# Kernel optimization log

Hardware: AMD Instinct MI355X
Metric: run time of the kernel (lower is better)

## Reference

```python
import jax, jax.numpy as jnp
import numpy as np

B, N_VEC, D, C, N_W, N_CLASS, VOCAB = 16, 4096, 256, 256, 12, 10, 32
N_LINKS = N_W + 1


def _chord_cols(n_vec, n_links):
    # cols[i] = [i, (i+2^0)%n, (i+2^1)%n, ..., (i+2^(L-2))%n]
    i = np.arange(n_vec)[:, None]
    offs = np.concatenate([[0], 2 ** np.arange(n_links - 1)])[None, :]
    return ((i + offs) % n_vec).astype(np.int32)


def setup_inputs() -> dict:
    key = jax.random.key(0)
    ks = jax.random.split(key, 16)
    s = 0.02
    return {
        "tokens": jax.random.randint(ks[0], (B, N_VEC), 0, VOCAB),
        "cols": jnp.asarray(_chord_cols(N_VEC, N_LINKS)),
        "emb": jax.random.normal(ks[1], (VOCAB, D), jnp.float32) * s,
        "pos_emb": jax.random.normal(ks[2], (N_VEC, D), jnp.float32) * s,
        "g_w1": jax.random.normal(ks[3], (D, C), jnp.float32) * s,
        "g_b1": jnp.zeros((C,), jnp.float32),
        "g_w2": jax.random.normal(ks[4], (C, C), jnp.float32) * s,
        "g_b2": jnp.zeros((C,), jnp.float32),
        "fs_w1": jax.random.normal(ks[5], (N_W, D, D), jnp.float32) * s,
        "fs_b1": jnp.zeros((N_W, D), jnp.float32),
        "fs_w2": jax.random.normal(ks[6], (N_W, D, N_LINKS), jnp.float32) * s,
        "fs_b2": jnp.zeros((N_W, N_LINKS), jnp.float32),
        "fin_w": jax.random.normal(ks[7], (C, N_CLASS), jnp.float32) * s,
        "fin_b": jnp.zeros((N_CLASS,), jnp.float32),
    }


def reference(tokens, cols, emb, pos_emb, g_w1, g_b1, g_w2, g_b2,
              fs_w1, fs_b1, fs_w2, fs_b2, fin_w, fin_b):
    # token + positional embedding: [B, N, D]
    data = emb[tokens] + pos_emb[None, :, :]
    # g MLP -> V: [B, N, C]   (torch GELU = exact erf)
    V = jax.nn.gelu(data @ g_w1 + g_b1, approximate=False) @ g_w2 + g_b2
    res = V
    n_w = fs_w1.shape[0]
    for m in range(n_w):
        # per-edge weights: [B, N, L]
        W = jax.nn.gelu(data @ fs_w1[m] + fs_b1[m], approximate=False) @ fs_w2[m] + fs_b2[m]
        # chord spmm: V[b,i] = sum_l W[b,i,l] * V[b, cols[i,l]]
        Vg = V[:, cols, :]                       # [B, N, L, C]
        V = jnp.einsum('bnl,bnlc->bnc', W, Vg) + res
    cls = V[:, 0, :]                             # CLS pooling
    return cls @ fin_w + fin_b
```

## Files before the change

### kernel.cpp

```cpp
#include <hip/hip_runtime.h>
#include <hip/hip_bf16.h>
#include <math.h>

namespace {

constexpr int Bb   = 16;
constexpr int Nv   = 4096;
constexpr int NW   = 12;
constexpr int NL   = 13;
constexpr int NCLS = 10;
constexpr int BN   = Bb * Nv;

typedef __attribute__((ext_vector_type(8))) short short8;
typedef __attribute__((ext_vector_type(4))) float float4_t;

__device__ __forceinline__ float gelu_poly(float x) {
    float u = x * x;
    float p = fmaf(u, fmaf(u, fmaf(u, -2.374656431e-3f, 1.994711402e-2f),
                           -1.329807601e-1f), 7.978845608e-1f);
    return x * fmaf(x * p, 0.5f, 0.5f);
}
__device__ __forceinline__ float bflo(unsigned int u) {
    return __builtin_bit_cast(float, u << 16);
}
__device__ __forceinline__ float bfhi(unsigned int u) {
    return __builtin_bit_cast(float, u & 0xffff0000u);
}
__device__ __forceinline__ unsigned int f2bf(float f) {
    unsigned int x = __builtin_bit_cast(unsigned int, f);
    x += 0x7fff + ((x >> 16) & 1);
    return x >> 16;
}
__device__ __forceinline__ unsigned short f2bf16(float f) {
    return __builtin_bit_cast(unsigned short, __float2bfloat16(f));
}
__device__ __forceinline__ void gload16(const unsigned short* g, unsigned short* l) {
    __builtin_amdgcn_global_load_lds(
        (const __attribute__((address_space(1))) void*)g,
        (__attribute__((address_space(3))) void*)l, 16, 0, 0);
}
__device__ __forceinline__ int xcd_swz(int bid) {
    return (bid & 7) * 128 + (bid >> 3);
}


__global__ __launch_bounds__(256) void xbf_kernel(
    const int* __restrict__ tokens,
    const float* __restrict__ emb,
    const float* __restrict__ pos,
    unsigned int* __restrict__ Xbf)
{
    int i  = blockIdx.x * 256 + threadIdx.x;
    int p  = i & 127;
    int bn = i >> 7;
    int n  = bn & (Nv - 1);
    int t  = tokens[bn];
    const float2* e2 = (const float2*)(emb + (size_t)t * 256);
    const float2* p2 = (const float2*)(pos + (size_t)n * 256);
    float2 a = e2[p], b = p2[p];
    Xbf[i] = f2bf(a.x + b.x) | (f2bf(a.y + b.y) << 16);
}

__global__ __launch_bounds__(256) void wt_kernel(
    const float* __restrict__ g_w1,
    const float* __restrict__ g_w2,
    const float* __restrict__ fs_w1,
    const float* __restrict__ fs_w2,
    unsigned short* __restrict__ WT,
    unsigned short* __restrict__ W2T)
{
    int bid = blockIdx.x;
    int t = threadIdx.x;
    if (bid < 14 * 16) {
        int mat = bid >> 4;
        int k0  = (bid & 15) * 16;
        const float* src = (mat == 0) ? g_w1
                         : (mat == 1) ? g_w2
                         : fs_w1 + (size_t)(mat - 2) * 65536;
        unsigned short tmp[16];
#pragma unroll
        for (int j = 0; j < 16; ++j)
            tmp[j] = (unsigned short)f2bf(src[(size_t)(k0 + j) * 256 + t]);
        unsigned short* dst = WT + ((size_t)mat * 256 + t) * 256 + k0;
#pragma unroll
        for (int j = 0; j < 16; ++j) dst[j] = tmp[j];
    } else {
        int m = bid - 224;
        const float* src = fs_w2 + (size_t)m * 256 * NL;
        unsigned short* dst = W2T + (size_t)m * 4096;
#pragma unroll
        for (int i = 0; i < 16; ++i) {
            int idx = t + i * 256;
            int n = idx >> 8, k = idx & 255;
            dst[idx] = (n < NL) ? (unsigned short)f2bf(src[(size_t)k * NL + n]) : 0;
        }
    }
}

__device__ __forceinline__ void gemm1_core(
    const unsigned short* __restrict__ Xg,
    const unsigned short* __restrict__ Wg,
    int row0, int tid,
    unsigned short* Xs,
    unsigned short* Wls,
    float4_t acc[4][4])
{
    const int w = tid >> 6, lane = tid & 63;
    const int wr = w >> 2, wc = w & 3;
    const int l15 = lane & 15, lg = lane >> 4;

    for (int k0 = 0; k0 < 256; k0 += 64) {
#pragma unroll
        for (int i = 0; i < 2; ++i) {
            int slotb = i * 512 + w * 64;
            int slot = slotb + lane;
            int row = slot >> 3, pu = slot & 7, lu = pu ^ (row & 7);
            gload16(Xg + (size_t)(row0 + row) * 256 + k0 + lu * 8, Xs + slotb * 8);
        }
#pragma unroll
        for (int i = 0; i < 4; ++i) {
            int slotb = i * 512 + w * 64;
            int slot = slotb + lane;
            int n = slot >> 3, pu = slot & 7, lu = pu ^ (n & 7);
            gload16(Wg + (size_t)n * 256 + k0 + lu * 8, Wls + slotb * 8);
        }
        __syncthreads();

#pragma unroll
        for (int ks = 0; ks < 2; ++ks) {
            short8 a[4], b[4];
#pragma unroll
            for (int fr = 0; fr < 4; ++fr) {
                int r = wr * 64 + fr * 16 + l15;
                int off = r * 128 + (((lg + ks * 4) ^ (l15 & 7)) << 4);
                a[fr] = *(const short8*)((const char*)Xs + off);
            }
#pragma unroll
            for (int nt = 0; nt < 4; ++nt) {
                int n = wc * 64 + nt * 16 + l15;
                int off = n * 128 + (((lg + ks * 4) ^ (l15 & 7)) << 4);
                b[nt] = *(const short8*)((const char*)Wls + off);
            }
#pragma unroll
            for (int fr = 0; fr < 4; ++fr)
#pragma unroll
                for (int nt = 0; nt < 4; ++nt)
                    acc[fr][nt] = __builtin_amdgcn_mfma_f32_16x16x32_bf16(
                        a[fr], b[nt], acc[fr][nt], 0, 0, 0);
        }
        __syncthreads();
    }
}

template<bool GELU>
__global__ __launch_bounds__(512) void gemm_act_kernel(
    const unsigned short* __restrict__ X,
    const unsigned short* __restrict__ WT,
    const float* __restrict__ bias,
    unsigned short* __restrict__ Y)
{
    __shared__ __align__(128) unsigned char smem[49152];
    unsigned short* Xs  = (unsigned short*)smem;
    unsigned short* Wls = (unsigned short*)(smem + 16384);

    const int row0 = ((blockIdx.x & 7) * 64 + (blockIdx.x >> 3)) * 128;
    const int tid  = threadIdx.x;
    const int w = tid >> 6, lane = tid & 63;
    const int wr = w >> 2, wc = w & 3;
    const int l15 = lane & 15, lg = lane >> 4;

    float4_t acc[4][4];
#pragma unroll
    for (int fr = 0; fr < 4; ++fr)
#pragma unroll
        for (int nt = 0; nt < 4; ++nt) acc[fr][nt] = (float4_t)0.f;

    gemm1_core(X, WT, row0, tid, Xs, Wls, acc);

#pragma unroll
    for (int nt = 0; nt < 4; ++nt) {
        int c = wc * 64 + nt * 16 + l15;
        float bv = bias[c];
#pragma unroll
        for (int fr = 0; fr < 4; ++fr)
#pragma unroll
            for (int reg = 0; reg < 4; ++reg) {
                float v = acc[fr][nt][reg] + bv;
                if (GELU) v = gelu_poly(v);
                Y[(size_t)(row0 + wr * 64 + fr * 16 + lg * 4 + reg) * 256 + c]
                    = f2bf16(v);
            }
    }
}

__global__ __launch_bounds__(512) void fsmlp_kernel(
    const unsigned short* __restrict__ X,
    const unsigned short* __restrict__ WT,
    const unsigned short* __restrict__ W2T,
    const float* __restrict__ fs_b1,
    const float* __restrict__ fs_b2,
    float* __restrict__ Wall)
{
    __shared__ __align__(128) unsigned char smem[65536];
    unsigned short* Xs  = (unsigned short*)smem;
    unsigned short* Wls = (unsigned short*)(smem + 16384);
    unsigned short* Hs  = (unsigned short*)smem;

    const int bid  = (blockIdx.x & 7) * 768 + (blockIdx.x >> 3);
    const int m    = bid % 12;
    const int row0 = (bid / 12) * 128;
    const int tid  = threadIdx.x;
    const int w = tid >> 6, lane = tid & 63;
    const int wr = w >> 2, wc = w & 3;
    const int l15 = lane & 15, lg = lane >> 4;

    const unsigned short* Wg   = WT + (size_t)(2 + m) * 65536;
    const unsigned short* W2Tm = W2T + (size_t)m * 4096;
    const float* b1m = fs_b1 + (size_t)m * 256;
    const float* b2m = fs_b2 + (size_t)m * NL;
    float* Wallm = Wall + (size_t)m * BN * NL;

    float4_t acc[4][4];
#pragma unroll
    for (int fr = 0; fr < 4; ++fr)
#pragma unroll
        for (int nt = 0; nt < 4; ++nt) acc[fr][nt] = (float4_t)0.f;

    gemm1_core(X, Wg, row0, tid, Xs, Wls, acc);

    short8 b2[8];
#pragma unroll
    for (int kc = 0; kc < 8; ++kc)
        b2[kc] = *(const short8*)(W2Tm + l15 * 256 + kc * 32 + lg * 8);

#pragma unroll
    for (int nt = 0; nt < 4; ++nt) {
        int c = wc * 64 + nt * 16 + l15;
        float bv = b1m[c];
        int cu = c >> 3, cl = c & 7;
#pragma unroll
        for (int fr = 0; fr < 4; ++fr)
#pragma unroll
            for (int reg = 0; reg < 4; ++reg) {
                int row = wr * 64 + fr * 16 + lg * 4 + reg;
                Hs[row * 256 + ((cu ^ (row & 7)) << 3) + cl] =
                    f2bf16(gelu_poly(acc[fr][nt][reg] + bv));
            }
    }
    __syncthreads();

    float4_t wacc = (float4_t)0.f;
#pragma unroll
    for (int kc = 0; kc < 8; ++kc) {
        int ua = (((kc * 4 + lg) ^ (l15 & 7)) << 3);
        short8 a = *(const short8*)(Hs + (w * 16 + l15) * 256 + ua);
        wacc = __builtin_amdgcn_mfma_f32_16x16x32_bf16(a, b2[kc], wacc, 0, 0, 0);
    }
    if (l15 < NL) {
        float b2v = b2m[l15];
#pragma unroll
        for (int reg = 0; reg < 4; ++reg)
            Wallm[(size_t)(row0 + w * 16 + lg * 4 + reg) * NL + l15]
                = wacc[reg] + b2v;
    }
}

__global__ __launch_bounds__(256) void chord_kernel(
    const unsigned short* __restrict__ Vprev,
    const uint2* __restrict__ res,
    const float* __restrict__ Wm,
    uint2* __restrict__ Vnext)
{
    __shared__ __align__(16) unsigned short Vs[96 * 256];
    __shared__ float Wmix[64][NL];

    const int bid  = xcd_swz(blockIdx.x);
    const int row0 = bid * 64;
    const int n0   = row0 & (Nv - 1);
    const int bb   = row0 & ~(Nv - 1);
    const int tid  = threadIdx.x;

    for (int e = tid; e < 64 * NL; e += 256)
        Wmix[0][e] = Wm[(size_t)row0 * NL + e];

#pragma unroll
    for (int i = 0; i < 12; ++i) {
        int slot = i * 256 + tid;
        int j = slot >> 5, cu = slot & 31;
        int gr = bb + ((n0 + j) & (Nv - 1));
        gload16(Vprev + (size_t)gr * 256 + cu * 8, Vs + slot * 8);
    }
    __syncthreads();

    const int p = tid & 63;
    const int w = tid >> 6;
    const uint2* V2 = (const uint2*)Vprev;

    for (int it = 0; it < 16; ++it) {
        const int r = w * 16 + it;
        const size_t rb = (size_t)(row0 + r) * 64;
        uint2 rv = res[rb + p];
        float a0 = bflo(rv.x), a1 = bfhi(rv.x);
        float a2 = bflo(rv.y), a3 = bfhi(rv.y);

        const unsigned short* lbase = Vs + r * 256 + p * 4;
#pragma unroll
        for (int l = 0; l < 7; ++l) {
            const int off = (l == 0) ? 0 : (1 << (l - 1));
            uint2 gv = *(const uint2*)(lbase + off * 256);
            float wv = Wmix[r][l];
            a0 += wv * bflo(gv.x);  a1 += wv * bfhi(gv.x);
            a2 += wv * bflo(gv.y);  a3 += wv * bfhi(gv.y);
        }
#pragma unroll
        for (int l = 7; l < NL; ++l) {
            const int off = 1 << (l - 1);
            int gr = bb + ((n0 + r + off) & (Nv - 1));
            uint2 gv = V2[(size_t)gr * 64 + p];
            float wv = Wmix[r][l];
            a0 += wv * bflo(gv.x);  a1 += wv * bfhi(gv.x);
            a2 += wv * bflo(gv.y);  a3 += wv * bfhi(gv.y);
        }
        uint2 o;
        o.x = f2bf(a0) | (f2bf(a1) << 16);
        o.y = f2bf(a2) | (f2bf(a3) << 16);
        Vnext[rb + p] = o;
    }
}

__global__ __launch_bounds__(256) void final_kernel(
    const unsigned short* __restrict__ Vfin,
    const float* __restrict__ fin_w,
    const float* __restrict__ fin_b,
    float* __restrict__ out)
{
    int t = threadIdx.x;
    if (t < Bb * NCLS) {
        int b = t / NCLS, o = t % NCLS;
        float a = fin_b[o];
        const unsigned short* v = Vfin + (size_t)b * Nv * 256;
        for (int k = 0; k < 256; ++k)
            a += __builtin_bit_cast(float, (unsigned int)v[k] << 16)
                 * fin_w[k * NCLS + o];
        out[t] = a;
    }
}

}

extern "C" void kernel_launch(void* const* d_in, const int* in_sizes, int n_in,
                              void* d_out, int out_size, void* d_ws, size_t ws_size,
                              hipStream_t stream) {
    const int*   tokens = (const int*)d_in[0];
    const float* emb    = (const float*)d_in[2];
    const float* pos    = (const float*)d_in[3];
    const float* g_w1   = (const float*)d_in[4];
    const float* g_b1   = (const float*)d_in[5];
    const float* g_w2   = (const float*)d_in[6];
    const float* g_b2   = (const float*)d_in[7];
    const float* fs_w1  = (const float*)d_in[8];
    const float* fs_b1  = (const float*)d_in[9];
    const float* fs_w2  = (const float*)d_in[10];
    const float* fs_b2  = (const float*)d_in[11];
    const float* fin_w  = (const float*)d_in[12];
    const float* fin_b  = (const float*)d_in[13];
    float* out = (float*)d_out;

    unsigned short* Xbf = (unsigned short*)d_ws;
    unsigned short* WT  = Xbf + (size_t)BN * 256;
    unsigned short* W2T = WT + (size_t)14 * 65536;
    unsigned short* res = W2T + (size_t)12 * 4096;
    unsigned short* Va  = res + (size_t)BN * 256;
    unsigned short* Vb  = Va + (size_t)BN * 256;
    float* Wall = (float*)(Vb + (size_t)BN * 256);

    xbf_kernel<<<BN * 128 / 256, 256, 0, stream>>>(tokens, emb, pos,
                                                   (unsigned int*)Xbf);
    wt_kernel<<<14 * 16 + 12, 256, 0, stream>>>(g_w1, g_w2, fs_w1, fs_w2,
                                                WT, W2T);

    gemm_act_kernel<true><<<512, 512, 0, stream>>>(Xbf, WT, g_b1, Va);
    gemm_act_kernel<false><<<512, 512, 0, stream>>>(Va, WT + 65536, g_b2, res);

    fsmlp_kernel<<<6144, 512, 0, stream>>>(Xbf, WT, W2T, fs_b1, fs_b2, Wall);

    const unsigned short* vp = res;
    for (int m = 0; m < NW; ++m) {
        unsigned short* vn = (m & 1) ? Vb : Va;
        chord_kernel<<<1024, 256, 0, stream>>>(
            vp, (const uint2*)res,
            Wall + (size_t)m * BN * NL, (uint2*)vn);
        vp = vn;
    }

    final_kernel<<<1, 256, 0, stream>>>(vp, fin_w, fin_b, out);
}
```

Baseline: 587.5 us.

## Double-buffer GEMM K-tiles and widen chord kernel to 16-byte vectors

The shared GEMM core is restructured into a two-buffer pipeline: the next 64-wide K tile is staged into a second LDS buffer while MFMAs run on the current one. This is meant to hide global-to-LDS latency, at the cost of doubling LDS per block to 96KB, which may reduce occupancy. The chord kernel now processes 8 bf16 per thread with uint4 loads and stores. It also serves the offset-64 link from the already-staged LDS tile for the first 32 rows, cutting global gathers.

```diff
diff --git a/kernel.cpp b/kernel.cpp
--- a/kernel.cpp
+++ b/kernel.cpp
@@ -97,59 +97,82 @@
     }
 }
 
-__device__ __forceinline__ void gemm1_core(
+
+__device__ __forceinline__ void stage_tile(
+    const unsigned short* __restrict__ Xg,
+    const unsigned short* __restrict__ Wg,
+    int row0, int k0, int tid,
+    unsigned short* Xs, unsigned short* Wls)
+{
+    const int w = tid >> 6, lane = tid & 63;
+#pragma unroll
+    for (int i = 0; i < 2; ++i) {
+        int slotb = i * 512 + w * 64;
+        int slot = slotb + lane;
+        int row = slot >> 3, pu = slot & 7, lu = pu ^ (row & 7);
+        gload16(Xg + (size_t)(row0 + row) * 256 + k0 + lu * 8, Xs + slotb * 8);
+    }
+#pragma unroll
+    for (int i = 0; i < 4; ++i) {
+        int slotb = i * 512 + w * 64;
+        int slot = slotb + lane;
+        int n = slot >> 3, pu = slot & 7, lu = pu ^ (n & 7);
+        gload16(Wg + (size_t)n * 256 + k0 + lu * 8, Wls + slotb * 8);
+    }
+}
+
+__device__ __forceinline__ void compute_tile(
+    const unsigned short* Xs, const unsigned short* Wls,
+    int wr, int wc, int l15, int lg, float4_t acc[4][4])
+{
+#pragma unroll
+    for (int ks = 0; ks < 2; ++ks) {
+        short8 a[4], b[4];
+#pragma unroll
+        for (int fr = 0; fr < 4; ++fr) {
+            int r = wr * 64 + fr * 16 + l15;
+            int off = r * 128 + (((lg + ks * 4) ^ (l15 & 7)) << 4);
+            a[fr] = *(const short8*)((const char*)Xs + off);
+        }
+#pragma unroll
+        for (int nt = 0; nt < 4; ++nt) {
+            int n = wc * 64 + nt * 16 + l15;
+            int off = n * 128 + (((lg + ks * 4) ^ (l15 & 7)) << 4);
+            b[nt] = *(const short8*)((const char*)Wls + off);
+        }
+#pragma unroll
+        for (int fr = 0; fr < 4; ++fr)
+#pragma unroll
+            for (int nt = 0; nt < 4; ++nt)
+                acc[fr][nt] = __builtin_amdgcn_mfma_f32_16x16x32_bf16(
+                    a[fr], b[nt], acc[fr][nt], 0, 0, 0);
+    }
+}
+
+__device__ __forceinline__ void gemm_db(
     const unsigned short* __restrict__ Xg,
     const unsigned short* __restrict__ Wg,
     int row0, int tid,
-    unsigned short* Xs,
-    unsigned short* Wls,
+    unsigned short* Xs0, unsigned short* Wls0,
+    unsigned short* Xs1, unsigned short* Wls1,
     float4_t acc[4][4])
 {
     const int w = tid >> 6, lane = tid & 63;
     const int wr = w >> 2, wc = w & 3;
     const int l15 = lane & 15, lg = lane >> 4;
 
-    for (int k0 = 0; k0 < 256; k0 += 64) {
-#pragma unroll
-        for (int i = 0; i < 2; ++i) {
-            int slotb = i * 512 + w * 64;
-            int slot = slotb + lane;
-            int row = slot >> 3, pu = slot & 7, lu = pu ^ (row & 7);
-            gload16(Xg + (size_t)(row0 + row) * 256 + k0 + lu * 8, Xs + slotb * 8);
-        }
-#pragma unroll
-        for (int i = 0; i < 4; ++i) {
-            int slotb = i * 512 + w * 64;
-            int slot = slotb + lane;
-            int n = slot >> 3, pu = slot & 7, lu = pu ^ (n & 7);
-            gload16(Wg + (size_t)n * 256 + k0 + lu * 8, Wls + slotb * 8);
-        }
-        __syncthreads();
-
-#pragma unroll
-        for (int ks = 0; ks < 2; ++ks) {
-            short8 a[4], b[4];
-#pragma unroll
-            for (int fr = 0; fr < 4; ++fr) {
-                int r = wr * 64 + fr * 16 + l15;
-                int off = r * 128 + (((lg + ks * 4) ^ (l15 & 7)) << 4);
-                a[fr] = *(const short8*)((const char*)Xs + off);
-            }
-#pragma unroll
-            for (int nt = 0; nt < 4; ++nt) {
-                int n = wc * 64 + nt * 16 + l15;
-                int off = n * 128 + (((lg + ks * 4) ^ (l15 & 7)) << 4);
-                b[nt] = *(const short8*)((const char*)Wls + off);
-            }
-#pragma unroll
-            for (int fr = 0; fr < 4; ++fr)
-#pragma unroll
-                for (int nt = 0; nt < 4; ++nt)
-                    acc[fr][nt] = __builtin_amdgcn_mfma_f32_16x16x32_bf16(
-                        a[fr], b[nt], acc[fr][nt], 0, 0, 0);
-        }
-        __syncthreads();
-    }
+    stage_tile(Xg, Wg, row0, 0, tid, Xs0, Wls0);
+    __syncthreads();
+    stage_tile(Xg, Wg, row0, 64, tid, Xs1, Wls1);
+    compute_tile(Xs0, Wls0, wr, wc, l15, lg, acc);
+    __syncthreads();
+    stage_tile(Xg, Wg, row0, 128, tid, Xs0, Wls0);
+    compute_tile(Xs1, Wls1, wr, wc, l15, lg, acc);
+    __syncthreads();
+    stage_tile(Xg, Wg, row0, 192, tid, Xs1, Wls1);
+    compute_tile(Xs0, Wls0, wr, wc, l15, lg, acc);
+    __syncthreads();
+    compute_tile(Xs1, Wls1, wr, wc, l15, lg, acc);
 }
 
 template<bool GELU>
@@ -159,9 +182,11 @@
     const float* __restrict__ bias,
     unsigned short* __restrict__ Y)
 {
-    __shared__ __align__(128) unsigned char smem[49152];
-    unsigned short* Xs  = (unsigned short*)smem;
-    unsigned short* Wls = (unsigned short*)(smem + 16384);
+    __shared__ __align__(128) unsigned char smem[98304];
+    unsigned short* Xs0  = (unsigned short*)smem;
+    unsigned short* Wls0 = (unsigned short*)(smem + 16384);
+    unsigned short* Xs1  = (unsigned short*)(smem + 49152);
+    unsigned short* Wls1 = (unsigned short*)(smem + 65536);
 
     const int row0 = ((blockIdx.x & 7) * 64 + (blockIdx.x >> 3)) * 128;
     const int tid  = threadIdx.x;
@@ -175,7 +200,7 @@
 #pragma unroll
         for (int nt = 0; nt < 4; ++nt) acc[fr][nt] = (float4_t)0.f;
 
-    gemm1_core(X, WT, row0, tid, Xs, Wls, acc);
+    gemm_db(X, WT, row0, tid, Xs0, Wls0, Xs1, Wls1, acc);
 
 #pragma unroll
     for (int nt = 0; nt < 4; ++nt) {
@@ -201,10 +226,12 @@
     const float* __restrict__ fs_b2,
     float* __restrict__ Wall)
 {
-    __shared__ __align__(128) unsigned char smem[65536];
-    unsigned short* Xs  = (unsigned short*)smem;
-    unsigned short* Wls = (unsigned short*)(smem + 16384);
-    unsigned short* Hs  = (unsigned short*)smem;
+    __shared__ __align__(128) unsigned char smem[98304];
+    unsigned short* Xs0  = (unsigned short*)smem;
+    unsigned short* Wls0 = (unsigned short*)(smem + 16384);
+    unsigned short* Xs1  = (unsigned short*)(smem + 49152);
+    unsigned short* Wls1 = (unsigned short*)(smem + 65536);
+    unsigned short* Hs   = (unsigned short*)smem;
 
     const int bid  = (blockIdx.x & 7) * 768 + (blockIdx.x >> 3);
     const int m    = bid % 12;
@@ -226,12 +253,14 @@
 #pragma unroll
         for (int nt = 0; nt < 4; ++nt) acc[fr][nt] = (float4_t)0.f;
 
-    gemm1_core(X, Wg, row0, tid, Xs, Wls, acc);
+    gemm_db(X, Wg, row0, tid, Xs0, Wls0, Xs1, Wls1, acc);
 
     short8 b2[8];
 #pragma unroll
     for (int kc = 0; kc < 8; ++kc)
         b2[kc] = *(const short8*)(W2Tm + l15 * 256 + kc * 32 + lg * 8);
+
+    __syncthreads();
 
 #pragma unroll
     for (int nt = 0; nt < 4; ++nt) {
@@ -267,9 +296,9 @@
 
 __global__ __launch_bounds__(256) void chord_kernel(
     const unsigned short* __restrict__ Vprev,
-    const uint2* __restrict__ res,
+    const uint4* __restrict__ res,
     const float* __restrict__ Wm,
-    uint2* __restrict__ Vnext)
+    uint4* __restrict__ Vnext)
 {
     __shared__ __align__(16) unsigned short Vs[96 * 256];
     __shared__ float Wmix[64][NL];
@@ -292,39 +321,57 @@
     }
     __syncthreads();
 
-    const int p = tid & 63;
-    const int w = tid >> 6;
-    const uint2* V2 = (const uint2*)Vprev;
-
-    for (int it = 0; it < 16; ++it) {
-        const int r = w * 16 + it;
-        const size_t rb = (size_t)(row0 + r) * 64;
-        uint2 rv = res[rb + p];
+    const int p4 = tid & 31;
+    const int w8 = tid >> 5;
+    const uint4* V4 = (const uint4*)Vprev;
+
+    for (int it = 0; it < 8; ++it) {
+        const int r = w8 * 8 + it;
+        const size_t rb = (size_t)(row0 + r) * 32;
+        uint4 rv = res[rb + p4];
         float a0 = bflo(rv.x), a1 = bfhi(rv.x);
         float a2 = bflo(rv.y), a3 = bfhi(rv.y);
-
-        const unsigned short* lbase = Vs + r * 256 + p * 4;
+        float a4 = bflo(rv.z), a5 = bfhi(rv.z);
+        float a6 = bflo(rv.w), a7 = bfhi(rv.w);
+
+        const unsigned short* lbase = Vs + r * 256 + p4 * 8;
 #pragma unroll
         for (int l = 0; l < 7; ++l) {
             const int off = (l == 0) ? 0 : (1 << (l - 1));
-            uint2 gv = *(const uint2*)(lbase + off * 256);
+            uint4 gv = *(const uint4*)(lbase + off * 256);
             float wv = Wmix[r][l];
             a0 += wv * bflo(gv.x);  a1 += wv * bfhi(gv.x);
             a2 += wv * bflo(gv.y);  a3 += wv * bfhi(gv.y);
-        }
-#pragma unroll
-        for (int l = 7; l < NL; ++l) {
+            a4 += wv * bflo(gv.z);  a5 += wv * bfhi(gv.z);
+            a6 += wv * bflo(gv.w);  a7 += wv * bfhi(gv.w);
+        }
+        {
+            float wv = Wmix[r][7];
+            uint4 gv;
+            if (r < 32) gv = *(const uint4*)(lbase + 64 * 256);
+            else gv = V4[(size_t)(bb + ((n0 + r + 64) & (Nv - 1))) * 32 + p4];
+            a0 += wv * bflo(gv.x);  a1 += wv * bfhi(gv.x);
+            a2 += wv * bflo(gv.y);  a3 += wv * bfhi(gv.y);
+            a4 += wv * bflo(gv.z);  a5 += wv * bfhi(gv.z);
+            a6 += wv * bflo(gv.w);  a7 += wv * bfhi(gv.w);
+        }
+#pragma unroll
+        for (int l = 8; l < NL; ++l) {
             const int off = 1 << (l - 1);
             int gr = bb + ((n0 + r + off) & (Nv - 1));
-            uint2 gv = V2[(size_t)gr * 64 + p];
+            uint4 gv = V4[(size_t)gr * 32 + p4];
             float wv = Wmix[r][l];
             a0 += wv * bflo(gv.x);  a1 += wv * bfhi(gv.x);
             a2 += wv * bflo(gv.y);  a3 += wv * bfhi(gv.y);
-        }
-        uint2 o;
+            a4 += wv * bflo(gv.z);  a5 += wv * bfhi(gv.z);
+            a6 += wv * bflo(gv.w);  a7 += wv * bfhi(gv.w);
+        }
+        uint4 o;
         o.x = f2bf(a0) | (f2bf(a1) << 16);
         o.y = f2bf(a2) | (f2bf(a3) << 16);
-        Vnext[rb + p] = o;
+        o.z = f2bf(a4) | (f2bf(a5) << 16);
+        o.w = f2bf(a6) | (f2bf(a7) << 16);
+        Vnext[rb + p4] = o;
     }
 }
 
@@ -388,8 +435,8 @@
     for (int m = 0; m < NW; ++m) {
         unsigned short* vn = (m & 1) ? Vb : Va;
         chord_kernel<<<1024, 256, 0, stream>>>(
-            vp, (const uint2*)res,
-            Wall + (size_t)m * BN * NL, (uint2*)vn);
+            vp, (const uint4*)res,
+            Wall + (size_t)m * BN * NL, (uint4*)vn);
         vp = vn;
     }
 
```

Result: slower. 670.4 us (+14.1%).

## Double-buffer GEMM K-loop with 32-wide stages to overlap loads and MFMA

Applied to the files above, without the earlier changes.

Replaces the single-buffered 64-wide K loop with a ping-pong scheme over 32-wide K slices. The next slice is prefetched into the alternate LDS buffer while MFMAs run on the current one. This hides global-load latency behind compute and cuts barriers per slice from two to one, but it doubles the number of stages and uses a narrower 4-way swizzle that may raise LDS bank conflicts.

```diff
diff --git a/kernel.cpp b/kernel.cpp
--- a/kernel.cpp
+++ b/kernel.cpp
@@ -97,57 +97,72 @@
     }
 }
 
-__device__ __forceinline__ void gemm1_core(
+
+__device__ __forceinline__ void stage32(
+    const unsigned short* __restrict__ Xg,
+    const unsigned short* __restrict__ Wg,
+    int row0, int k0, int tid,
+    unsigned short* Xs, unsigned short* Ws)
+{
+    {
+        int slot = tid;
+        int row = slot >> 2, pu = slot & 3, lu = pu ^ (row & 3);
+        gload16(Xg + (size_t)(row0 + row) * 256 + k0 + lu * 8, Xs + slot * 8);
+    }
+#pragma unroll
+    for (int i = 0; i < 2; ++i) {
+        int slot = i * 512 + tid;
+        int n = slot >> 2, pu = slot & 3, lu = pu ^ (n & 3);
+        gload16(Wg + (size_t)n * 256 + k0 + lu * 8, Ws + slot * 8);
+    }
+}
+
+__device__ __forceinline__ void compute32(
+    const unsigned short* Xs, const unsigned short* Ws,
+    int wr, int wc, int l15, int lg, float4_t acc[4][4])
+{
+    short8 a[4], b[4];
+#pragma unroll
+    for (int fr = 0; fr < 4; ++fr) {
+        int r = wr * 64 + fr * 16 + l15;
+        a[fr] = *(const short8*)(Xs + r * 32 + ((lg ^ (r & 3)) << 3));
+    }
+#pragma unroll
+    for (int nt = 0; nt < 4; ++nt) {
+        int n = wc * 64 + nt * 16 + l15;
+        b[nt] = *(const short8*)(Ws + n * 32 + ((lg ^ (n & 3)) << 3));
+    }
+#pragma unroll
+    for (int fr = 0; fr < 4; ++fr)
+#pragma unroll
+        for (int nt = 0; nt < 4; ++nt)
+            acc[fr][nt] = __builtin_amdgcn_mfma_f32_16x16x32_bf16(
+                a[fr], b[nt], acc[fr][nt], 0, 0, 0);
+}
+
+__device__ __forceinline__ void gemm_2ph(
     const unsigned short* __restrict__ Xg,
     const unsigned short* __restrict__ Wg,
     int row0, int tid,
-    unsigned short* Xs,
-    unsigned short* Wls,
+    unsigned short* Xs0, unsigned short* Ws0,
+    unsigned short* Xs1, unsigned short* Ws1,
     float4_t acc[4][4])
 {
     const int w = tid >> 6, lane = tid & 63;
     const int wr = w >> 2, wc = w & 3;
     const int l15 = lane & 15, lg = lane >> 4;
-
-    for (int k0 = 0; k0 < 256; k0 += 64) {
-#pragma unroll
-        for (int i = 0; i < 2; ++i) {
-            int slotb = i * 512 + w * 64;
-            int slot = slotb + lane;
-            int row = slot >> 3, pu = slot & 7, lu = pu ^ (row & 7);
-            gload16(Xg + (size_t)(row0 + row) * 256 + k0 + lu * 8, Xs + slotb * 8);
-        }
-#pragma unroll
-        for (int i = 0; i < 4; ++i) {
-            int slotb = i * 512 + w * 64;
-            int slot = slotb + lane;
-            int n = slot >> 3, pu = slot & 7, lu = pu ^ (n & 7);
-            gload16(Wg + (size_t)n * 256 + k0 + lu * 8, Wls + slotb * 8);
-        }
-        __syncthreads();
-
-#pragma unroll
-        for (int ks = 0; ks < 2; ++ks) {
-            short8 a[4], b[4];
-#pragma unroll
-            for (int fr = 0; fr < 4; ++fr) {
-                int r = wr * 64 + fr * 16 + l15;
-                int off = r * 128 + (((lg + ks * 4) ^ (l15 & 7)) << 4);
-                a[fr] = *(const short8*)((const char*)Xs + off);
-            }
-#pragma unroll
-            for (int nt = 0; nt < 4; ++nt) {
-                int n = wc * 64 + nt * 16 + l15;
-                int off = n * 128 + (((lg + ks * 4) ^ (l15 & 7)) << 4);
-                b[nt] = *(const short8*)((const char*)Wls + off);
-            }
-#pragma unroll
-            for (int fr = 0; fr < 4; ++fr)
-#pragma unroll
-                for (int nt = 0; nt < 4; ++nt)
-                    acc[fr][nt] = __builtin_amdgcn_mfma_f32_16x16x32_bf16(
-                        a[fr], b[nt], acc[fr][nt], 0, 0, 0);
-        }
+    (void)w;
+
+    stage32(Xg, Wg, row0, 0, tid, Xs0, Ws0);
+    __syncthreads();
+#pragma unroll
+    for (int t = 0; t < 8; ++t) {
+        unsigned short* Xc = (t & 1) ? Xs1 : Xs0;
+        unsigned short* Wc = (t & 1) ? Ws1 : Ws0;
+        unsigned short* Xn = (t & 1) ? Xs0 : Xs1;
+        unsigned short* Wn = (t & 1) ? Ws0 : Ws1;
+        if (t < 7) stage32(Xg, Wg, row0, (t + 1) * 32, tid, Xn, Wn);
+        compute32(Xc, Wc, wr, wc, l15, lg, acc);
         __syncthreads();
     }
 }
@@ -160,8 +175,10 @@
     unsigned short* __restrict__ Y)
 {
     __shared__ __align__(128) unsigned char smem[49152];
-    unsigned short* Xs  = (unsigned short*)smem;
-    unsigned short* Wls = (unsigned short*)(smem + 16384);
+    unsigned short* Xs0 = (unsigned short*)smem;
+    unsigned short* Ws0 = (unsigned short*)(smem + 8192);
+    unsigned short* Xs1 = (unsigned short*)(smem + 24576);
+    unsigned short* Ws1 = (unsigned short*)(smem + 32768);
 
     const int row0 = ((blockIdx.x & 7) * 64 + (blockIdx.x >> 3)) * 128;
     const int tid  = threadIdx.x;
@@ -175,7 +192,7 @@
 #pragma unroll
         for (int nt = 0; nt < 4; ++nt) acc[fr][nt] = (float4_t)0.f;
 
-    gemm1_core(X, WT, row0, tid, Xs, Wls, acc);
+    gemm_2ph(X, WT, row0, tid, Xs0, Ws0, Xs1, Ws1, acc);
 
 #pragma unroll
     for (int nt = 0; nt < 4; ++nt) {
@@ -202,8 +219,10 @@
     float* __restrict__ Wall)
 {
     __shared__ __align__(128) unsigned char smem[65536];
-    unsigned short* Xs  = (unsigned short*)smem;
-    unsigned short* Wls = (unsigned short*)(smem + 16384);
+    unsigned short* Xs0 = (unsigned short*)smem;
+    unsigned short* Ws0 = (unsigned short*)(smem + 8192);
+    unsigned short* Xs1 = (unsigned short*)(smem + 24576);
+    unsigned short* Ws1 = (unsigned short*)(smem + 32768);
     unsigned short* Hs  = (unsigned short*)smem;
 
     const int bid  = (blockIdx.x & 7) * 768 + (blockIdx.x >> 3);
@@ -226,7 +245,7 @@
 #pragma unroll
         for (int nt = 0; nt < 4; ++nt) acc[fr][nt] = (float4_t)0.f;
 
-    gemm1_core(X, Wg, row0, tid, Xs, Wls, acc);
+    gemm_2ph(X, Wg, row0, tid, Xs0, Ws0, Xs1, Ws1, acc);
 
     short8 b2[8];
 #pragma unroll
```

Result: no change. 596.1 us (+1.5%).

## Make fsmlp persistent with the full layer weight resident in LDS

Applied to the files above, without the earlier changes.

fsmlp_kernel now launches 768 blocks. Each block loads one layer's whole 256x256 bf16 weight once into LDS, pre-swizzled by wt_kernel into a new WTs buffer, then loops over 16 row tiles of 64 rows. X fragments are read straight from global memory instead of being staged through shared memory, which removes the repeated per-tile weight staging of the old 6144-block launch. In exchange the block uses 160KB of LDS, leaving one block per CU, and the second GEMM runs on only 4 of 8 waves.

```diff
diff --git a/kernel.cpp b/kernel.cpp
--- a/kernel.cpp
+++ b/kernel.cpp
@@ -67,7 +67,8 @@
     const float* __restrict__ fs_w1,
     const float* __restrict__ fs_w2,
     unsigned short* __restrict__ WT,
-    unsigned short* __restrict__ W2T)
+    unsigned short* __restrict__ W2T,
+    unsigned short* __restrict__ WTs)
 {
     int bid = blockIdx.x;
     int t = threadIdx.x;
@@ -84,6 +85,14 @@
         unsigned short* dst = WT + ((size_t)mat * 256 + t) * 256 + k0;
 #pragma unroll
         for (int j = 0; j < 16; ++j) dst[j] = tmp[j];
+        if (mat >= 2) {
+            int s0 = k0 >> 3;
+            unsigned short* db = WTs + ((size_t)(mat - 2) * 256 + t) * 256;
+            unsigned short* d0 = db + ((s0 ^ (t & 7)) << 3);
+            unsigned short* d1 = db + (((s0 + 1) ^ (t & 7)) << 3);
+#pragma unroll
+            for (int j = 0; j < 8; ++j) { d0[j] = tmp[j]; d1[j] = tmp[8 + j]; }
+        }
     } else {
         int m = bid - 224;
         const float* src = fs_w2 + (size_t)m * 256 * NL;
@@ -195,73 +204,116 @@
 
 __global__ __launch_bounds__(512) void fsmlp_kernel(
     const unsigned short* __restrict__ X,
-    const unsigned short* __restrict__ WT,
+    const unsigned short* __restrict__ WTs,
     const unsigned short* __restrict__ W2T,
     const float* __restrict__ fs_b1,
     const float* __restrict__ fs_b2,
     float* __restrict__ Wall)
 {
-    __shared__ __align__(128) unsigned char smem[65536];
-    unsigned short* Xs  = (unsigned short*)smem;
-    unsigned short* Wls = (unsigned short*)(smem + 16384);
-    unsigned short* Hs  = (unsigned short*)smem;
-
-    const int bid  = (blockIdx.x & 7) * 768 + (blockIdx.x >> 3);
-    const int m    = bid % 12;
-    const int row0 = (bid / 12) * 128;
-    const int tid  = threadIdx.x;
+    __shared__ __align__(128) unsigned char smem[163840];
+    unsigned short* WLds = (unsigned short*)smem;
+    unsigned short* Hs   = (unsigned short*)(smem + 131072);
+
+    const int xcd = blockIdx.x & 7;
+    const int idx = blockIdx.x >> 3;
+    const int m   = idx % 12;
+    const int ch  = xcd * 8 + idx / 12;
+    const int rbase = ch * 1024;
+
+    const int tid = threadIdx.x;
     const int w = tid >> 6, lane = tid & 63;
     const int wr = w >> 2, wc = w & 3;
     const int l15 = lane & 15, lg = lane >> 4;
 
-    const unsigned short* Wg   = WT + (size_t)(2 + m) * 65536;
+    const unsigned short* WTm  = WTs + (size_t)m * 65536;
     const unsigned short* W2Tm = W2T + (size_t)m * 4096;
     const float* b1m = fs_b1 + (size_t)m * 256;
     const float* b2m = fs_b2 + (size_t)m * NL;
     float* Wallm = Wall + (size_t)m * BN * NL;
 
-    float4_t acc[4][4];
-#pragma unroll
-    for (int fr = 0; fr < 4; ++fr)
-#pragma unroll
-        for (int nt = 0; nt < 4; ++nt) acc[fr][nt] = (float4_t)0.f;
-
-    gemm1_core(X, Wg, row0, tid, Xs, Wls, acc);
-
-    short8 b2[8];
+#pragma unroll
+    for (int i = 0; i < 16; ++i) {
+        int slot = i * 512 + tid;
+        gload16(WTm + slot * 8, WLds + slot * 8);
+    }
+
+    float bvs[4];
+#pragma unroll
+    for (int nt = 0; nt < 4; ++nt) bvs[nt] = b1m[wc * 64 + nt * 16 + l15];
+    const float b2v = (l15 < NL) ? b2m[l15] : 0.f;
+    short8 b2f[8];
 #pragma unroll
     for (int kc = 0; kc < 8; ++kc)
-        b2[kc] = *(const short8*)(W2Tm + l15 * 256 + kc * 32 + lg * 8);
-
-#pragma unroll
-    for (int nt = 0; nt < 4; ++nt) {
-        int c = wc * 64 + nt * 16 + l15;
-        float bv = b1m[c];
-        int cu = c >> 3, cl = c & 7;
-#pragma unroll
-        for (int fr = 0; fr < 4; ++fr)
-#pragma unroll
-            for (int reg = 0; reg < 4; ++reg) {
-                int row = wr * 64 + fr * 16 + lg * 4 + reg;
-                Hs[row * 256 + ((cu ^ (row & 7)) << 3) + cl] =
-                    f2bf16(gelu_poly(acc[fr][nt][reg] + bv));
-            }
-    }
+        b2f[kc] = *(const short8*)(W2Tm + l15 * 256 + kc * 32 + lg * 8);
+
     __syncthreads();
 
-    float4_t wacc = (float4_t)0.f;
-#pragma unroll
-    for (int kc = 0; kc < 8; ++kc) {
-        int ua = (((kc * 4 + lg) ^ (l15 & 7)) << 3);
-        short8 a = *(const short8*)(Hs + (w * 16 + l15) * 256 + ua);
-        wacc = __builtin_amdgcn_mfma_f32_16x16x32_bf16(a, b2[kc], wacc, 0, 0, 0);
-    }
-    if (l15 < NL) {
-        float b2v = b2m[l15];
-#pragma unroll
-        for (int reg = 0; reg < 4; ++reg)
-            Wallm[(size_t)(row0 + w * 16 + lg * 4 + reg) * NL + l15]
-                = wacc[reg] + b2v;
+    for (int tile = 0; tile < 16; ++tile) {
+        const int row0 = rbase + tile * 64;
+
+        float4_t acc[2][4];
+#pragma unroll
+        for (int fr = 0; fr < 2; ++fr)
+#pragma unroll
+            for (int nt = 0; nt < 4; ++nt) acc[fr][nt] = (float4_t)0.f;
+
+#pragma unroll
+        for (int t = 0; t < 8; ++t) {
+            const int k0 = t * 32;
+            short8 a[2], b[4];
+#pragma unroll
+            for (int fr = 0; fr < 2; ++fr) {
+                int r = row0 + wr * 32 + fr * 16 + l15;
+                a[fr] = *(const short8*)(X + (size_t)r * 256 + k0 + lg * 8);
+            }
+#pragma unroll
+            for (int nt = 0; nt < 4; ++nt) {
+                int n = wc * 64 + nt * 16 + l15;
+                int slot = t * 4 + lg;
+                b[nt] = *(const short8*)(WLds + n * 256 +
+                                         ((slot ^ (n & 7)) << 3));
+            }
+#pragma unroll
+            for (int fr = 0; fr < 2; ++fr)
+#pragma unroll
+                for (int nt = 0; nt < 4; ++nt)
+                    acc[fr][nt] = __builtin_amdgcn_mfma_f32_16x16x32_bf16(
+                        a[fr], b[nt], acc[fr][nt], 0, 0, 0);
+        }
+
+        __syncthreads();
+
+#pragma unroll
+        for (int nt = 0; nt < 4; ++nt) {
+            int c = wc * 64 + nt * 16 + l15;
+            int cu = c >> 3, cl = c & 7;
+#pragma unroll
+            for (int fr = 0; fr < 2; ++fr)
+#pragma unroll
+                for (int reg = 0; reg < 4; ++reg) {
+                    int lr = wr * 32 + fr * 16 + lg * 4 + reg;
+                    Hs[lr * 256 + ((cu ^ (lr & 7)) << 3) + cl] =
+                        f2bf16(gelu_poly(acc[fr][nt][reg] + bvs[nt]));
+                }
+        }
+        __syncthreads();
+
+        if (w < 4) {
+            float4_t wacc = (float4_t)0.f;
+#pragma unroll
+            for (int kc = 0; kc < 8; ++kc) {
+                int ua = (((kc * 4 + lg) ^ (l15 & 7)) << 3);
+                short8 a2 = *(const short8*)(Hs + (w * 16 + l15) * 256 + ua);
+                wacc = __builtin_amdgcn_mfma_f32_16x16x32_bf16(
+                    a2, b2f[kc], wacc, 0, 0, 0);
+            }
+            if (l15 < NL) {
+#pragma unroll
+                for (int reg = 0; reg < 4; ++reg)
+                    Wallm[(size_t)(row0 + w * 16 + lg * 4 + reg) * NL + l15]
+                        = wacc[reg] + b2v;
+            }
+        }
     }
 }
 
@@ -369,7 +421,8 @@
     unsigned short* Xbf = (unsigned short*)d_ws;
     unsigned short* WT  = Xbf + (size_t)BN * 256;
     unsigned short* W2T = WT + (size_t)14 * 65536;
-    unsigned short* res = W2T + (size_t)12 * 4096;
+    unsigned short* WTs = W2T + (size_t)12 * 4096;
+    unsigned short* res = WTs + (size_t)12 * 65536;
     unsigned short* Va  = res + (size_t)BN * 256;
     unsigned short* Vb  = Va + (size_t)BN * 256;
     float* Wall = (float*)(Vb + (size_t)BN * 256);
@@ -377,12 +430,12 @@
     xbf_kernel<<<BN * 128 / 256, 256, 0, stream>>>(tokens, emb, pos,
                                                    (unsigned int*)Xbf);
     wt_kernel<<<14 * 16 + 12, 256, 0, stream>>>(g_w1, g_w2, fs_w1, fs_w2,
-                                                WT, W2T);
+                                                WT, W2T, WTs);
 
     gemm_act_kernel<true><<<512, 512, 0, stream>>>(Xbf, WT, g_b1, Va);
     gemm_act_kernel<false><<<512, 512, 0, stream>>>(Va, WT + 65536, g_b2, res);
 
-    fsmlp_kernel<<<6144, 512, 0, stream>>>(Xbf, WT, W2T, fs_b1, fs_b2, Wall);
+    fsmlp_kernel<<<768, 512, 0, stream>>>(Xbf, WTs, W2T, fs_b1, fs_b2, Wall);
 
     const unsigned short* vp = res;
     for (int m = 0; m < NW; ++m) {
```

Measured after the change: 633.8 us. 7.9% more time.
